# Performance work log

Hardware: AMD Instinct MI355X
Metric: run time of the kernel (lower is better)

Reference implementation:

```python
import jax, jax.numpy as jnp
import numpy as np
from jax import lax

T, N, E, B = 8, 50000, 100000, 512
DN = DE = DG = 128


def _linear_params(key, d_in, d_out):
    k1, k2 = jax.random.split(key)
    s = 1.0 / float(np.sqrt(d_in))
    W = jax.random.uniform(k1, (d_in, d_out), minval=-s, maxval=s, dtype=jnp.float32)
    b = jax.random.uniform(k2, (d_out,), minval=-s, maxval=s, dtype=jnp.float32)
    return W, b


def setup_inputs() -> dict:
    key = jax.random.key(0)
    ks = jax.random.split(key, 12)
    inp = {
        "xs": jax.random.normal(ks[0], (T, N, DN), dtype=jnp.float32),
        "es": jax.random.normal(ks[1], (T, E, DE), dtype=jnp.float32),
        "gs": jax.random.normal(ks[2], (T, B, DG), dtype=jnp.float32),
    }
    i = 3
    for name, d in (("node", DN), ("edge", DE), ("glob", DG)):
        W1, b1 = _linear_params(ks[i], 2 * d, d)  # sig1 sees cat(prev_out, x_t)
        W2, b2 = _linear_params(ks[i + 1], d, d)
        W3, b3 = _linear_params(ks[i + 2], d, d)
        i += 3
        inp[f"W1_{name}"], inp[f"b1_{name}"] = W1, b1
        inp[f"W2_{name}"], inp[f"b2_{name}"] = W2, b2
        inp[f"W3_{name}"], inp[f"b3_{name}"] = W3, b3
    return inp


def _run_component(seq, W1, b1, W2, b2, W3, b3):
    # seq: [T, M, d]; recurrent LSTM-style gating per element, fused in a scan.
    def step(carry, x_t):
        state, out = carry
        forget = jax.nn.sigmoid(jnp.concatenate([out, x_t], axis=-1) @ W1 + b1)
        state = state * forget + jax.nn.sigmoid(x_t @ W2 + b2) * jnp.tanh(x_t)
        out = jnp.tanh(state) * jax.nn.sigmoid(x_t @ W3 + b3)
        return (state, out), None

    (state, out), _ = lax.scan(step, (seq[0], seq[0]), seq)
    return state, out


def reference(xs, es, gs,
              W1_node, b1_node, W2_node, b2_node, W3_node, b3_node,
              W1_edge, b1_edge, W2_edge, b2_edge, W3_edge, b3_edge,
              W1_glob, b1_glob, W2_glob, b2_glob, W3_glob, b3_glob):
    sx, ox = _run_component(xs, W1_node, b1_node, W2_node, b2_node, W3_node, b3_node)
    se, oe = _run_component(es, W1_edge, b1_edge, W2_edge, b2_edge, W3_edge, b3_edge)
    sg, og = _run_component(gs, W1_glob, b1_glob, W2_glob, b2_glob, W3_glob, b3_glob)
    # (state, data) per component: node, edge, glob
    return (sx, se, sg, ox, oe, og)
```

## Files before the change

### kernel.cpp

```cpp
#include <hip/hip_runtime.h>

typedef __attribute__((ext_vector_type(8))) short bf16x8;
typedef __attribute__((ext_vector_type(4))) float f32x4;
typedef __attribute__((ext_vector_type(4))) short s16x4;

__device__ __forceinline__ unsigned cvt_pk(float lo, float hi) {
  unsigned r;
  asm("v_cvt_pk_bf16_f32 %0, %1, %2" : "=v"(r) : "v"(lo), "v"(hi));
  return r;
}
__device__ __forceinline__ float bf2f(short s) {
  return __uint_as_float(((unsigned)(unsigned short)s) << 16);
}

#define LOG2E  1.4426950408889634f
#define LOG2E2 2.8853900817779268f

#define WS_MAT 32768
#define WS_COMP 131072
#define NODE_BLOCKS 3125
#define EDGE_BLOCKS 6250
#define GLOB_BLOCKS 32
#define NBLOCKS (NODE_BLOCKS + EDGE_BLOCKS + GLOB_BLOCKS)

#define SWZ(row, byte) ((row) * 256 + ((byte) ^ (((row) & 7) << 4)))
#define XBUF_B 4096
#define OBUF_B 4096
#define BIAS_OFF 20480
#define SMEM_B 22016

__global__ __launch_bounds__(256) void prep_weights(
    const float* __restrict__ W1, const float* __restrict__ W2,
    const float* __restrict__ W3, unsigned char* __restrict__ wsc) {
  const int m = blockIdx.x;
  const float* src; int rowoff = 0;
  if (m == 0)      { src = W1; }
  else if (m == 1) { src = W1; rowoff = 128; }
  else if (m == 2) { src = W2; }
  else             { src = W3; }
  short* dst = (short*)(wsc + (size_t)m * WS_MAT);
  for (int fi = threadIdx.x; fi < 2048; fi += 256) {
    int w = fi >> 8, kc = (fi >> 6) & 3, lane = fi & 63;
    int cc = lane & 15, gg = lane >> 4;
    int wcol = 16 * w + cc;
    int kb = 32 * kc + 8 * gg + rowoff;
    union { bf16x8 h; unsigned u[4]; } v;
#pragma unroll
    for (int j = 0; j < 4; ++j)
      v.u[j] = cvt_pk(src[(size_t)(kb + 2 * j) * 128 + wcol],
                      src[(size_t)(kb + 2 * j + 1) * 128 + wcol]);
    *(bf16x8*)(dst + (size_t)fi * 8) = v.h;
  }
}

__device__ __forceinline__ void pre_tile(
    const char* xb, const float* blds, int row, int g, int w,
    const bf16x8* w1b, const bf16x8* w2, const bf16x8* w3,
    f32x4& u, f32x4& g3, f32x4& aAx) {
  bf16x8 xf[4];
#pragma unroll
  for (int kc = 0; kc < 4; ++kc)
    xf[kc] = *(const bf16x8*)(xb + SWZ(row, 64 * kc + 16 * g));
  s16x4 xe4 = *(const s16x4*)(xb + SWZ(row, 32 * w + 8 * g));
  const int bo = 16 * w + 4 * g;
  f32x4 aX = *(const f32x4*)(blds + bo);
  f32x4 aB = *(const f32x4*)(blds + 128 + bo);
  f32x4 aC = *(const f32x4*)(blds + 256 + bo);
#pragma unroll
  for (int kc = 0; kc < 4; ++kc) {
    aX = __builtin_amdgcn_mfma_f32_16x16x32_bf16(w1b[kc], xf[kc], aX, 0, 0, 0);
    aB = __builtin_amdgcn_mfma_f32_16x16x32_bf16(w2[kc],  xf[kc], aB, 0, 0, 0);
    aC = __builtin_amdgcn_mfma_f32_16x16x32_bf16(w3[kc],  xf[kc], aC, 0, 0, 0);
  }
#pragma unroll
  for (int ri = 0; ri < 4; ++ri) {
    float A = __builtin_amdgcn_exp2f(LOG2E  * aB[ri]);
    float E = __builtin_amdgcn_exp2f(LOG2E2 * bf2f(xe4[ri]));
    u[ri]  = (A * (E - 1.f)) * __builtin_amdgcn_rcpf((1.f + A) * (E + 1.f));
    g3[ri] = __builtin_amdgcn_rcpf(1.f + __builtin_amdgcn_exp2f(-LOG2E * aC[ri]));
  }
  aAx = aX;
}

__device__ __forceinline__ void ser_tile(
    const char* ofsrc, char* obw, bool wr, int row, int g, int w,
    const bf16x8* w1a, f32x4 aAx, f32x4 u, f32x4 g3, f32x4& st) {
  bf16x8 of[4];
#pragma unroll
  for (int kc = 0; kc < 4; ++kc)
    of[kc] = *(const bf16x8*)(ofsrc + SWZ(row, 64 * kc + 16 * g));
  f32x4 aA1 = aAx;
  f32x4 aA2 = (f32x4){0.f, 0.f, 0.f, 0.f};
  aA1 = __builtin_amdgcn_mfma_f32_16x16x32_bf16(w1a[0], of[0], aA1, 0, 0, 0);
  aA2 = __builtin_amdgcn_mfma_f32_16x16x32_bf16(w1a[2], of[2], aA2, 0, 0, 0);
  aA1 = __builtin_amdgcn_mfma_f32_16x16x32_bf16(w1a[1], of[1], aA1, 0, 0, 0);
  aA2 = __builtin_amdgcn_mfma_f32_16x16x32_bf16(w1a[3], of[3], aA2, 0, 0, 0);
  f32x4 ov;
#pragma unroll
  for (int ri = 0; ri < 4; ++ri) {
    float aA = aA1[ri] + aA2[ri];
    float N = __builtin_amdgcn_exp2f(-LOG2E * aA);
    float fgt = __builtin_amdgcn_rcpf(1.f + N);
    st[ri] = st[ri] * fgt + u[ri];
    float T = __builtin_amdgcn_rcpf(1.f + __builtin_amdgcn_exp2f(LOG2E2 * st[ri]));
    ov[ri] = (1.f - 2.f * T) * g3[ri];
  }
  if (wr) {
    union { s16x4 v; unsigned uu[2]; } ob;
    ob.uu[0] = cvt_pk(ov[0], ov[1]);
    ob.uu[1] = cvt_pk(ov[2], ov[3]);
    *(s16x4*)(obw + SWZ(row, 32 * w + 8 * g)) = ob.v;
  }
}

__global__ __launch_bounds__(512, 4) void glstm(
    const float* __restrict__ xs, const float* __restrict__ es,
    const float* __restrict__ gs, const unsigned char* __restrict__ ws,
    const float* __restrict__ b1n, const float* __restrict__ b2n, const float* __restrict__ b3n,
    const float* __restrict__ b1e, const float* __restrict__ b2e, const float* __restrict__ b3e,
    const float* __restrict__ b1g, const float* __restrict__ b2g, const float* __restrict__ b3g,
    float* __restrict__ dout) {
  __shared__ __align__(16) unsigned char smem[SMEM_B];

  const int bid = blockIdx.x, tid = threadIdx.x;
  const float* X; const float *B1, *B2, *B3; float *S, *O; int M, unit, comp;
  if (bid < NODE_BLOCKS) {
    X = xs; M = 50000;  S = dout;              O = dout + 19265536L;
    unit = bid; comp = 0; B1 = b1n; B2 = b2n; B3 = b3n;
  } else if (bid < NODE_BLOCKS + EDGE_BLOCKS) {
    X = es; M = 100000; S = dout + 6400000L;   O = dout + 25665536L;
    unit = bid - NODE_BLOCKS; comp = 1; B1 = b1e; B2 = b2e; B3 = b3e;
  } else {
    X = gs; M = 512;    S = dout + 19200000L;  O = dout + 38465536L;
    unit = bid - (NODE_BLOCKS + EDGE_BLOCKS); comp = 2; B1 = b1g; B2 = b2g; B3 = b3g;
  }

  const int w = tid >> 6, l = tid & 63, c = l & 15, g = l >> 4;
  const int Ra = unit * 16;

  bf16x8 wA[4][4];
  {
    const short* wsrc = (const short*)(ws + (size_t)comp * WS_COMP);
#pragma unroll
    for (int m = 0; m < 4; ++m)
#pragma unroll
      for (int kc = 0; kc < 4; ++kc)
        wA[m][kc] = *(const bf16x8*)(wsrc + (size_t)m * 16384 + ((w * 4 + kc) * 64 + l) * 8);
  }

  char* xb0 = (char*)smem;
  char* xb1 = (char*)smem + XBUF_B;
  char* xb2 = (char*)smem + 2 * XBUF_B;
  char* ob0 = (char*)smem + 3 * XBUF_B;
  char* ob1 = (char*)smem + 3 * XBUF_B + OBUF_B;
  float* blds = (float*)(smem + BIAS_OFF);

  if (tid < 128) {
    blds[tid]       = B1[tid];
    blds[128 + tid] = B2[tid];
    blds[256 + tid] = B3[tid];
  }

  const int srow = tid >> 5;
  const int sbyte = (tid & 31) * 8;
  const int scol = (tid & 31) * 4;

  {
    const float* p0 = X + (size_t)(Ra + srow) * 128 + scol;
    const float* p1 = p0 + (size_t)M * 128;
    f32x4 a0 = *(const f32x4*)p0;
    f32x4 a1 = *(const f32x4*)p1;
    union { s16x4 v; unsigned u[2]; } o;
    o.u[0] = cvt_pk(a0[0], a0[1]); o.u[1] = cvt_pk(a0[2], a0[3]);
    *(s16x4*)(xb0 + SWZ(srow, sbyte)) = o.v;
    o.u[0] = cvt_pk(a1[0], a1[1]); o.u[1] = cvt_pk(a1[2], a1[3]);
    *(s16x4*)(xb1 + SWZ(srow, sbyte)) = o.v;
  }
  __syncthreads();

  f32x4 st, uu, g3, ax;
  {
    s16x4 e = *(const s16x4*)(xb0 + SWZ(c, 32 * w + 8 * g));
#pragma unroll
    for (int ri = 0; ri < 4; ++ri) st[ri] = bf2f(e[ri]);
  }
  pre_tile(xb0, blds, c, g, w, wA[1], wA[2], wA[3], uu, g3, ax);

  char* xr = xb1; char* xw = xb2; char* xsp = xb0;
  char* orf = ob0; char* owf = ob1;

#pragma unroll 1
  for (int t = 0; t < 8; ++t) {
    f32x4 pa;
    const bool pf = (t < 6);
    if (pf) {
      const float* p = X + ((size_t)(t + 2) * M + Ra + srow) * 128 + scol;
      pa = *(const f32x4*)p;
    }

    const char* ofs = (t == 0) ? (const char*)xsp : (const char*)orf;
    ser_tile(ofs, owf, t < 7, c, g, w, wA[0], ax, uu, g3, st);

    if (t < 7)
      pre_tile(xr, blds, c, g, w, wA[1], wA[2], wA[3], uu, g3, ax);

    if (pf) {
      union { s16x4 v; unsigned u[2]; } o;
      o.u[0] = cvt_pk(pa[0], pa[1]); o.u[1] = cvt_pk(pa[2], pa[3]);
      *(s16x4*)(xw + SWZ(srow, sbyte)) = o.v;
    }
    if (t < 7) __syncthreads();

    char* tx = xsp; xsp = xr; xr = xw; xw = tx;
    char* to = orf; orf = owf; owf = to;
  }

  {
    f32x4 ov;
#pragma unroll
    for (int ri = 0; ri < 4; ++ri) {
      float T = __builtin_amdgcn_rcpf(1.f + __builtin_amdgcn_exp2f(LOG2E2 * st[ri]));
      ov[ri] = (1.f - 2.f * T) * g3[ri];
    }
    size_t o = (size_t)(Ra + c) * 128 + 16 * w + 4 * g;
    *(f32x4*)(S + o) = st;
    *(f32x4*)(O + o) = ov;
  }
}

extern "C" void kernel_launch(void* const* d_in, const int* in_sizes, int n_in,
                              void* d_out, int out_size, void* d_ws, size_t ws_size,
                              hipStream_t stream) {
  (void)in_sizes; (void)n_in; (void)out_size; (void)ws_size;
  const float* xs = (const float*)d_in[0];
  const float* es = (const float*)d_in[1];
  const float* gs = (const float*)d_in[2];
  unsigned char* ws = (unsigned char*)d_ws;

  for (int comp = 0; comp < 3; ++comp) {
    const float* W1 = (const float*)d_in[3 + comp * 6 + 0];
    const float* W2 = (const float*)d_in[3 + comp * 6 + 2];
    const float* W3 = (const float*)d_in[3 + comp * 6 + 4];
    prep_weights<<<4, 256, 0, stream>>>(W1, W2, W3, ws + (size_t)comp * WS_COMP);
  }
  glstm<<<NBLOCKS, 512, 0, stream>>>(
      xs, es, gs, ws,
      (const float*)d_in[4],  (const float*)d_in[6],  (const float*)d_in[8],
      (const float*)d_in[10], (const float*)d_in[12], (const float*)d_in[14],
      (const float*)d_in[16], (const float*)d_in[18], (const float*)d_in[20],
      (float*)d_out);
}
```

Before: 290.9 us.

## Fold log2e scaling into weights/biases and pair reciprocals to cut transcendental ops

Pre-scales the bf16 weight matrices and LDS biases by ±log2(e), so the exp2 arguments come straight out of the MFMA accumulators without extra multiplies. Pairs reciprocals, computing 1/(a*b) once and recovering each with a multiply, which halves the rcp count. It also collapses the split accumulator chain in the serial step into one chain and skips the output tanh when the tile is not written. Together these cut transcendental and VALU work on the recurrent critical path, at the risk of overflow in the paired products and a longer serial MFMA dependency chain.

```diff
diff --git a/kernel.cpp b/kernel.cpp
--- a/kernel.cpp
+++ b/kernel.cpp
@@ -33,11 +33,11 @@
     const float* __restrict__ W1, const float* __restrict__ W2,
     const float* __restrict__ W3, unsigned char* __restrict__ wsc) {
   const int m = blockIdx.x;
-  const float* src; int rowoff = 0;
-  if (m == 0)      { src = W1; }
-  else if (m == 1) { src = W1; rowoff = 128; }
-  else if (m == 2) { src = W2; }
-  else             { src = W3; }
+  const float* src; int rowoff = 0; float sc;
+  if (m == 0)      { src = W1; sc = -LOG2E; }
+  else if (m == 1) { src = W1; rowoff = 128; sc = -LOG2E; }
+  else if (m == 2) { src = W2; sc =  LOG2E; }
+  else             { src = W3; sc = -LOG2E; }
   short* dst = (short*)(wsc + (size_t)m * WS_MAT);
   for (int fi = threadIdx.x; fi < 2048; fi += 256) {
     int w = fi >> 8, kc = (fi >> 6) & 3, lane = fi & 63;
@@ -47,8 +47,8 @@
     union { bf16x8 h; unsigned u[4]; } v;
 #pragma unroll
     for (int j = 0; j < 4; ++j)
-      v.u[j] = cvt_pk(src[(size_t)(kb + 2 * j) * 128 + wcol],
-                      src[(size_t)(kb + 2 * j + 1) * 128 + wcol]);
+      v.u[j] = cvt_pk(sc * src[(size_t)(kb + 2 * j) * 128 + wcol],
+                      sc * src[(size_t)(kb + 2 * j + 1) * 128 + wcol]);
     *(bf16x8*)(dst + (size_t)fi * 8) = v.h;
   }
 }
@@ -73,11 +73,23 @@
     aC = __builtin_amdgcn_mfma_f32_16x16x32_bf16(w3[kc],  xf[kc], aC, 0, 0, 0);
   }
 #pragma unroll
-  for (int ri = 0; ri < 4; ++ri) {
-    float A = __builtin_amdgcn_exp2f(LOG2E  * aB[ri]);
-    float E = __builtin_amdgcn_exp2f(LOG2E2 * bf2f(xe4[ri]));
-    u[ri]  = (A * (E - 1.f)) * __builtin_amdgcn_rcpf((1.f + A) * (E + 1.f));
-    g3[ri] = __builtin_amdgcn_rcpf(1.f + __builtin_amdgcn_exp2f(-LOG2E * aC[ri]));
+  for (int p = 0; p < 2; ++p) {
+    const int r0 = 2 * p, r1 = 2 * p + 1;
+    float A0 = __builtin_amdgcn_exp2f(aB[r0]);
+    float A1 = __builtin_amdgcn_exp2f(aB[r1]);
+    float E0 = __builtin_amdgcn_exp2f(LOG2E2 * bf2f(xe4[r0]));
+    float E1 = __builtin_amdgcn_exp2f(LOG2E2 * bf2f(xe4[r1]));
+    float du0 = (1.f + A0) * (E0 + 1.f);
+    float du1 = (1.f + A1) * (E1 + 1.f);
+    float ru = __builtin_amdgcn_rcpf(du0 * du1);
+    u[r0] = (A0 * (E0 - 1.f)) * (ru * du1);
+    u[r1] = (A1 * (E1 - 1.f)) * (ru * du0);
+    float C0 = __builtin_amdgcn_exp2f(aC[r0]);
+    float C1 = __builtin_amdgcn_exp2f(aC[r1]);
+    float dg0 = 1.f + C0, dg1 = 1.f + C1;
+    float rg = __builtin_amdgcn_rcpf(dg0 * dg1);
+    g3[r0] = rg * dg1;
+    g3[r1] = rg * dg0;
   }
   aAx = aX;
 }
@@ -89,23 +101,34 @@
 #pragma unroll
   for (int kc = 0; kc < 4; ++kc)
     of[kc] = *(const bf16x8*)(ofsrc + SWZ(row, 64 * kc + 16 * g));
-  f32x4 aA1 = aAx;
-  f32x4 aA2 = (f32x4){0.f, 0.f, 0.f, 0.f};
-  aA1 = __builtin_amdgcn_mfma_f32_16x16x32_bf16(w1a[0], of[0], aA1, 0, 0, 0);
-  aA2 = __builtin_amdgcn_mfma_f32_16x16x32_bf16(w1a[2], of[2], aA2, 0, 0, 0);
-  aA1 = __builtin_amdgcn_mfma_f32_16x16x32_bf16(w1a[1], of[1], aA1, 0, 0, 0);
-  aA2 = __builtin_amdgcn_mfma_f32_16x16x32_bf16(w1a[3], of[3], aA2, 0, 0, 0);
-  f32x4 ov;
-#pragma unroll
-  for (int ri = 0; ri < 4; ++ri) {
-    float aA = aA1[ri] + aA2[ri];
-    float N = __builtin_amdgcn_exp2f(-LOG2E * aA);
-    float fgt = __builtin_amdgcn_rcpf(1.f + N);
-    st[ri] = st[ri] * fgt + u[ri];
-    float T = __builtin_amdgcn_rcpf(1.f + __builtin_amdgcn_exp2f(LOG2E2 * st[ri]));
-    ov[ri] = (1.f - 2.f * T) * g3[ri];
-  }
+  f32x4 aA = aAx;
+#pragma unroll
+  for (int kc = 0; kc < 4; ++kc)
+    aA = __builtin_amdgcn_mfma_f32_16x16x32_bf16(w1a[kc], of[kc], aA, 0, 0, 0);
+  float N0 = __builtin_amdgcn_exp2f(aA[0]);
+  float N1 = __builtin_amdgcn_exp2f(aA[1]);
+  float N2 = __builtin_amdgcn_exp2f(aA[2]);
+  float N3 = __builtin_amdgcn_exp2f(aA[3]);
+  float d0 = 1.f + N0, d1 = 1.f + N1, d2 = 1.f + N2, d3 = 1.f + N3;
+  float rf01 = __builtin_amdgcn_rcpf(d0 * d1);
+  float rf23 = __builtin_amdgcn_rcpf(d2 * d3);
+  st[0] = st[0] * (rf01 * d1) + u[0];
+  st[1] = st[1] * (rf01 * d0) + u[1];
+  st[2] = st[2] * (rf23 * d3) + u[2];
+  st[3] = st[3] * (rf23 * d2) + u[3];
   if (wr) {
+    float E0 = __builtin_amdgcn_exp2f(LOG2E2 * st[0]);
+    float E1 = __builtin_amdgcn_exp2f(LOG2E2 * st[1]);
+    float E2 = __builtin_amdgcn_exp2f(LOG2E2 * st[2]);
+    float E3 = __builtin_amdgcn_exp2f(LOG2E2 * st[3]);
+    float t0 = 1.f + E0, t1 = 1.f + E1, t2 = 1.f + E2, t3 = 1.f + E3;
+    float rt01 = __builtin_amdgcn_rcpf(t0 * t1);
+    float rt23 = __builtin_amdgcn_rcpf(t2 * t3);
+    f32x4 ov;
+    ov[0] = (1.f - 2.f * (rt01 * t1)) * g3[0];
+    ov[1] = (1.f - 2.f * (rt01 * t0)) * g3[1];
+    ov[2] = (1.f - 2.f * (rt23 * t3)) * g3[2];
+    ov[3] = (1.f - 2.f * (rt23 * t2)) * g3[3];
     union { s16x4 v; unsigned uu[2]; } ob;
     ob.uu[0] = cvt_pk(ov[0], ov[1]);
     ob.uu[1] = cvt_pk(ov[2], ov[3]);
@@ -156,9 +179,9 @@
   float* blds = (float*)(smem + BIAS_OFF);
 
   if (tid < 128) {
-    blds[tid]       = B1[tid];
-    blds[128 + tid] = B2[tid];
-    blds[256 + tid] = B3[tid];
+    blds[tid]       = -LOG2E * B1[tid];
+    blds[128 + tid] =  LOG2E * B2[tid];
+    blds[256 + tid] = -LOG2E * B3[tid];
   }
 
   const int srow = tid >> 5;
@@ -216,12 +239,18 @@
   }
 
   {
+    float E0 = __builtin_amdgcn_exp2f(LOG2E2 * st[0]);
+    float E1 = __builtin_amdgcn_exp2f(LOG2E2 * st[1]);
+    float E2 = __builtin_amdgcn_exp2f(LOG2E2 * st[2]);
+    float E3 = __builtin_amdgcn_exp2f(LOG2E2 * st[3]);
+    float t0 = 1.f + E0, t1 = 1.f + E1, t2 = 1.f + E2, t3 = 1.f + E3;
+    float rt01 = __builtin_amdgcn_rcpf(t0 * t1);
+    float rt23 = __builtin_amdgcn_rcpf(t2 * t3);
     f32x4 ov;
-#pragma unroll
-    for (int ri = 0; ri < 4; ++ri) {
-      float T = __builtin_amdgcn_rcpf(1.f + __builtin_amdgcn_exp2f(LOG2E2 * st[ri]));
-      ov[ri] = (1.f - 2.f * T) * g3[ri];
-    }
+    ov[0] = (1.f - 2.f * (rt01 * t1)) * g3[0];
+    ov[1] = (1.f - 2.f * (rt01 * t0)) * g3[1];
+    ov[2] = (1.f - 2.f * (rt23 * t3)) * g3[2];
+    ov[3] = (1.f - 2.f * (rt23 * t2)) * g3[3];
     size_t o = (size_t)(Ra + c) * 128 + 16 * w + 4 * g;
     *(f32x4*)(S + o) = st;
     *(f32x4*)(O + o) = ov;
```

Result: no change. 290.1 us (-0.3%).
